# Optimization experiments

Measured on AMD Instinct MI355X. Metric: run time of the kernel, lower is better.

## Reference

```python
import jax, jax.numpy as jnp
import numpy as np

K = 3        # kernel size
PAD = 1      # padding
DG = 16      # deformable groups
MAXR = 10.0  # max_residue_magnitude


def _lrelu(x):
    return jnp.where(x >= 0, x, 0.1 * x)


def _conv3(x, w, b):
    y = jax.lax.conv_general_dilated(x, w, (1, 1), 'SAME',
                                     dimension_numbers=('NCHW', 'OIHW', 'NCHW'))
    return y + b[None, :, None, None]


def _deform_conv2d(x, offset, mask, weight, bias):
    # x: [B,Cin,H,W]; offset: [B,2*DG*K*K,H,W]; mask: [B,DG*K*K,H,W]
    B, Cin, H, W = x.shape
    Cout = weight.shape[0]
    G, Cg, K2 = DG, Cin // DG, K * K
    off = offset.reshape(B, G, K2, 2, H, W)
    dy, dx = off[:, :, :, 0], off[:, :, :, 1]
    ky = jnp.repeat(jnp.arange(K), K).astype(x.dtype)   # [K2]
    kx = jnp.tile(jnp.arange(K), K).astype(x.dtype)
    hh = jnp.arange(H, dtype=x.dtype)
    ww = jnp.arange(W, dtype=x.dtype)
    # sampling positions [B,G,K2,H,W]
    py = dy + ky[None, None, :, None, None] + hh[None, None, None, :, None] - PAD
    px = dx + kx[None, None, :, None, None] + ww[None, None, None, None, :] - PAD
    y0 = jnp.floor(py)
    x0 = jnp.floor(px)
    wy1 = py - y0
    wx1 = px - x0
    xf = x.reshape(B, G, Cg, H * W)

    def gather(yi, xi, wgt):
        valid = (yi >= 0) & (yi <= H - 1) & (xi >= 0) & (xi <= W - 1)
        idx = (jnp.clip(yi, 0, H - 1).astype(jnp.int32) * W
               + jnp.clip(xi, 0, W - 1).astype(jnp.int32)).reshape(B, G, -1)
        vals = jnp.take_along_axis(
            xf, jnp.broadcast_to(idx[:, :, None, :], (B, G, Cg, idx.shape[-1])), axis=3)
        vals = vals.reshape(B, G, Cg, K2, H, W)
        w = (wgt * valid.astype(x.dtype))[:, :, None]  # [B,G,1,K2,H,W]
        return vals * w

    s = (gather(y0, x0, (1 - wy1) * (1 - wx1))
         + gather(y0, x0 + 1, (1 - wy1) * wx1)
         + gather(y0 + 1, x0, wy1 * (1 - wx1))
         + gather(y0 + 1, x0 + 1, wy1 * wx1))
    s = s * mask.reshape(B, G, K2, H, W)[:, :, None]
    wr = weight.reshape(Cout, G, Cg, K2)
    out = jnp.einsum('ogck,bgckhw->bohw', wr, s)
    return out + bias[None, :, None, None]


def setup_inputs() -> dict:
    key = jax.random.key(0)
    ks = jax.random.split(key, 16)
    B, Cin, Cout, H, W = 4, 128, 64, 96, 96
    Coff = 3 * Cout + 4  # 196
    stdv = 1.0 / np.sqrt(Cin * K * K)
    inp = {
        'x': jax.random.normal(ks[0], (B, Cin, H, W), jnp.float32),
        'extra_feat': jax.random.normal(ks[1], (B, 3 * Cout, H, W), jnp.float32),
        'flow_1': jax.random.normal(ks[2], (B, 2, H, W), jnp.float32),
        'flow_2': jax.random.normal(ks[3], (B, 2, H, W), jnp.float32),
        'weight': jax.random.uniform(ks[4], (Cout, Cin, K, K), jnp.float32, -stdv, stdv),
        'bias': jax.random.normal(ks[5], (Cout,), jnp.float32) * 0.01,
        'ow0': jax.random.normal(ks[6], (Cout, Coff, K, K), jnp.float32) * 0.02,
        'ob0': jnp.zeros((Cout,), jnp.float32),
        'ow1': jax.random.normal(ks[7], (Cout, Cout, K, K), jnp.float32) * 0.02,
        'ob1': jnp.zeros((Cout,), jnp.float32),
        'ow2': jax.random.normal(ks[8], (Cout, Cout, K, K), jnp.float32) * 0.02,
        'ob2': jnp.zeros((Cout,), jnp.float32),
        'ow3': jax.random.normal(ks[9], (27 * DG, Cout, K, K), jnp.float32) * 0.01,
        'ob3': jnp.zeros((27 * DG,), jnp.float32),
    }
    return inp


def reference(x, extra_feat, flow_1, flow_2, weight, bias,
              ow0, ob0, ow1, ob1, ow2, ob2, ow3, ob3):
    feat = jnp.concatenate([extra_feat, flow_1, flow_2], axis=1)
    h = _lrelu(_conv3(feat, ow0, ob0))
    h = _lrelu(_conv3(h, ow1, ob1))
    h = _lrelu(_conv3(h, ow2, ob2))
    out = _conv3(h, ow3, ob3)
    o1, o2, m = jnp.split(out, 3, axis=1)
    offs = MAXR * jnp.tanh(jnp.concatenate([o1, o2], axis=1))
    off1, off2 = jnp.split(offs, 2, axis=1)
    off1 = off1 + jnp.tile(flow_1[:, ::-1], (1, off1.shape[1] // 2, 1, 1))
    off2 = off2 + jnp.tile(flow_2[:, ::-1], (1, off2.shape[1] // 2, 1, 1))
    offset = jnp.concatenate([off1, off2], axis=1)
    mask = jax.nn.sigmoid(m)
    return _deform_conv2d(x, offset, mask, weight, bias)
```

## Files before the change

kernel.cpp:

```cpp
#include <hip/hip_runtime.h>
#include <math.h>

#define HW 9216
#define Hh 96
#define Ww 96
#define PHW 9604

typedef __attribute__((ext_vector_type(8))) short bh8;
typedef __attribute__((ext_vector_type(4))) short bh4;
typedef __attribute__((ext_vector_type(4))) float f32x4;
typedef __attribute__((ext_vector_type(2))) float f32x2;
typedef __attribute__((ext_vector_type(4))) int i32x4;
union bh8i { bh8 v; i32x4 i; };

__device__ __forceinline__ short f2bf(float f) {
    union { float f; unsigned u; } v; v.f = f;
    unsigned r = v.u + 0x7FFFu + ((v.u >> 16) & 1u);
    return (short)(r >> 16);
}
__device__ __forceinline__ float bf2f(short s) {
    union { unsigned u; float f; } v; v.u = ((unsigned)(unsigned short)s) << 16;
    return v.f;
}
__device__ __forceinline__ float lo_bf(unsigned u) {
    union { unsigned u; float f; } v; v.u = u << 16; return v.f;
}
__device__ __forceinline__ float hi_bf(unsigned u) {
    union { unsigned u; float f; } v; v.u = u & 0xFFFF0000u; return v.f;
}
__device__ __forceinline__ unsigned pack_bf2(float lo, float hi) {
    union { float f; unsigned u; } a, b; a.f = lo; b.f = hi;
    unsigned ul = a.u + 0x7FFFu + ((a.u >> 16) & 1u);
    unsigned uh = b.u + 0x7FFFu + ((b.u >> 16) & 1u);
    return (ul >> 16) | (uh & 0xFFFF0000u);
}

__global__ void prep_misc(short* __restrict__ xpad1, short* __restrict__ hpa,
                          short* __restrict__ hpb, short* __restrict__ xdp,
                          const float* __restrict__ ow0, const float* __restrict__ ow1,
                          const float* __restrict__ ow2, const float* __restrict__ ow3,
                          const float* __restrict__ wd,
                          short* __restrict__ wb0, short* __restrict__ wb1,
                          short* __restrict__ wb2, short* __restrict__ wb3,
                          short* __restrict__ wbd) {
    int i = blockIdx.x * 256 + threadIdx.x;
    const int z1 = 4 * 388 * 224, z2 = 4 * 388 * 64;
    if (i < z1 + 2 * z2) {
        short* p; int C;
        if (i < z1) { p = xpad1; C = 224; }
        else if (i < z1 + z2) { p = hpa; C = 64; i -= z1; }
        else { p = hpb; C = 64; i -= z1 + z2; }
        int c = i % C;
        int r = i / C;
        int b = r / 388, pid = r - b * 388;
        int row, col;
        if (pid < 98)       { row = 0;  col = pid; }
        else if (pid < 196) { row = 97; col = pid - 98; }
        else if (pid < 292) { row = pid - 196 + 1; col = 0; }
        else                { row = pid - 292 + 1; col = 97; }
        p[((size_t)b * PHW + row * 98 + col) * C + c] = 0;
        return;
    }
    i -= z1 + 2 * z2;
    const int zr = 4 * 16 * 388 * 8;
    if (i < zr) {
        int c8 = i & 7;
        int r = i >> 3;
        int pid = r % 388;
        int bg = r / 388;
        int row, col;
        if (pid < 98)       { row = 0;  col = pid; }
        else if (pid < 196) { row = 97; col = pid - 98; }
        else if (pid < 292) { row = pid - 196 + 1; col = 0; }
        else                { row = pid - 292 + 1; col = 97; }
        xdp[((size_t)bg * PHW + row * 98 + col) * 8 + c8] = 0;
        return;
    }
    i -= zr;
    const int n0 = 64 * 9 * 224, n1 = 64 * 9 * 64, n3 = 448 * 9 * 64, nd = 64 * 1152;
    if (i < n0) {
        int co = i / (9 * 224); int r = i - co * (9 * 224);
        int tap = r / 224, ci = r - tap * 224;
        wb0[i] = f2bf(ci < 196 ? ow0[(co * 196 + ci) * 9 + tap] : 0.f);
        return;
    }
    i -= n0;
    if (i < n1) {
        int co = i / (9 * 64); int r = i - co * (9 * 64);
        int tap = r / 64, ci = r - tap * 64;
        wb1[i] = f2bf(ow1[(co * 64 + ci) * 9 + tap]);
        return;
    }
    i -= n1;
    if (i < n1) {
        int co = i / (9 * 64); int r = i - co * (9 * 64);
        int tap = r / 64, ci = r - tap * 64;
        wb2[i] = f2bf(ow2[(co * 64 + ci) * 9 + tap]);
        return;
    }
    i -= n1;
    if (i < n3) {
        int co = i / (9 * 64); int r = i - co * (9 * 64);
        int tap = r / 64, ci = r - tap * 64;
        wb3[i] = f2bf(co < 432 ? ow3[(co * 64 + ci) * 9 + tap] : 0.f);
        return;
    }
    i -= n3;
    if (i < nd) {
        int co = i / 1152, kd = i - co * 1152;
        int gt = kd >> 3, c = kd & 7;
        int g = gt / 9, tap = gt - g * 9;
        wbd[i] = f2bf(wd[(co * 128 + g * 8 + c) * 9 + tap]);
    }
}

__global__ void pack_all(const float* __restrict__ extra,
                         const float* __restrict__ f1,
                         const float* __restrict__ f2,
                         const float* __restrict__ x,
                         short* __restrict__ xp,
                         short* __restrict__ xdp) {
    __shared__ float t[32][33];
    const int tid = threadIdx.x, tx = tid & 31, ty = tid >> 5;
    const int pt = blockIdx.x, b = blockIdx.z;
    if (blockIdx.y < 7) {
        const int ct = blockIdx.y;
#pragma unroll
        for (int j = 0; j < 4; ++j) {
            int ch = ct * 32 + ty + j * 8;
            int p = pt * 32 + tx;
            float v = 0.f;
            if (ch < 192)      v = extra[(b * 192 + ch) * HW + p];
            else if (ch < 194) v = f1[(b * 2 + ch - 192) * HW + p];
            else if (ch < 196) v = f2[(b * 2 + ch - 194) * HW + p];
            t[ty + j * 8][tx] = v;
        }
        __syncthreads();
#pragma unroll
        for (int j = 0; j < 4; ++j) {
            int pr = ty + j * 8;
            int p = pt * 32 + pr;
            int r = p / 96, c = p - r * 96;
            xp[((size_t)b * PHW + (r + 1) * 98 + (c + 1)) * 224 + ct * 32 + tx] =
                f2bf(t[tx][pr]);
        }
    } else {
        const int ct = blockIdx.y - 7;
#pragma unroll
        for (int j = 0; j < 4; ++j) {
            int ch = ct * 32 + ty + j * 8;
            t[ty + j * 8][tx] = x[((size_t)b * 128 + ch) * HW + pt * 32 + tx];
        }
        __syncthreads();
        if (tid < 128) {
            int oct = tid >> 5, p = tid & 31;
            int g = ct * 4 + oct;
            int pix = pt * 32 + p;
            int r = pix / 96, c = pix - r * 96;
            bh8 v;
#pragma unroll
            for (int cc = 0; cc < 8; ++cc) v[cc] = f2bf(t[oct * 8 + cc][p]);
            *(bh8*)&xdp[(((size_t)b * 16 + g) * PHW + (r + 1) * 98 + (c + 1)) * 8] = v;
        }
    }
}

template<int CINP, int KCH>
__launch_bounds__(256)
__global__ void conv_mfma(const short* __restrict__ xp,
                          const short* __restrict__ wb,
                          const float* __restrict__ bias,
                          short* __restrict__ o1) {
    __shared__ __attribute__((aligned(16))) short smA[9 * 64 * 32];
    const int tid = threadIdx.x;
    const int lane = tid & 63, wv = tid >> 6;
    const int q = lane >> 4, l15 = lane & 15;
    const int b = blockIdx.y;
    const int pix0 = blockIdx.x * 64 + wv * 16;
    const int soh = pix0 / 96, sow = pix0 - (pix0 / 96) * 96;

    const short* bp = xp + ((size_t)b * PHW + soh * 98 + sow + l15) * CINP + q * 8;

    const int sco = tid >> 2, sqq = tid & 3;
    const short* wsrc = wb + (size_t)sco * (9 * CINP) + sqq * 8;

    f32x4 acc[4];
#pragma unroll
    for (int t = 0; t < 4; ++t) acc[t] = (f32x4){0.f, 0.f, 0.f, 0.f};

    for (int p = 0; p < KCH; ++p) {
        __syncthreads();
        bh8 wtmp[9];
#pragma unroll
        for (int tap = 0; tap < 9; ++tap)
            wtmp[tap] = *(const bh8*)(wsrc + tap * CINP + p * 32);
#pragma unroll
        for (int tap = 0; tap < 9; ++tap)
            *(bh8*)&smA[tap * 2048 + sco * 32 + sqq * 8] = wtmp[tap];
        __syncthreads();
#pragma unroll
        for (int tap = 0; tap < 9; ++tap) {
            const int ky = tap / 3, kx = tap - (tap / 3) * 3;
            bh8 bf = *(const bh8*)(bp + (ky * 98 + kx) * CINP + p * 32);
#pragma unroll
            for (int t = 0; t < 4; ++t) {
                bh8 af = *(const bh8*)&smA[tap * 2048 + (t * 16 + l15) * 32 + q * 8];
                acc[t] = __builtin_amdgcn_mfma_f32_16x16x32_bf16(af, bf, acc[t], 0, 0, 0);
            }
        }
    }

    size_t base = ((size_t)b * PHW + (soh + 1) * 98 + sow + l15 + 1) * 64;
#pragma unroll
    for (int t = 0; t < 4; ++t) {
        bh4 v4;
#pragma unroll
        for (int r = 0; r < 4; ++r) {
            int co = t * 16 + q * 4 + r;
            float v = acc[t][r] + bias[co];
            v = (v >= 0.f) ? v : 0.1f * v;
            v4[r] = f2bf(v);
        }
        *(bh4*)(o1 + base + t * 16 + q * 4) = v4;
    }
}

__launch_bounds__(256)
__global__ void conv4_gemm(const short* __restrict__ xp,
                           const short* __restrict__ wb,
                           const float* __restrict__ bias,
                           float* __restrict__ offp,
                           short* __restrict__ maskb,
                           const float* __restrict__ flow1,
                           const float* __restrict__ flow2) {
    __shared__ __attribute__((aligned(16))) short smA[64 * 64];
    __shared__ __attribute__((aligned(16))) short smB[192 * 64];
    const int tid = threadIdx.x;
    const int lane = tid & 63, wv = tid >> 6;
    const int q = lane >> 4, l15 = lane & 15;
    const int pg = blockIdx.x;
    const int b = blockIdx.y;
    const int cob = blockIdx.z * 64;
    const int r0 = pg * 2;

    f32x4 acc[3][4];
#pragma unroll
    for (int pf = 0; pf < 3; ++pf)
#pragma unroll
        for (int cf = 0; cf < 4; ++cf) acc[pf][cf] = (f32x4){0.f, 0.f, 0.f, 0.f};

    for (int tap = 0; tap < 9; ++tap) {
        const int ky = tap / 3, kx = tap - (tap / 3) * 3;
        __syncthreads();
#pragma unroll
        for (int it = 0; it < 2; ++it) {
            int id = it * 256 + tid;
            int row = id >> 3, s = id & 7;
            int sw = s ^ (row & 7);
            *(bh8*)&smA[row * 64 + sw * 8] =
                *(const bh8*)(wb + (size_t)(cob + row) * 576 + tap * 64 + s * 8);
        }
#pragma unroll
        for (int it = 0; it < 6; ++it) {
            int id = it * 256 + tid;
            int row = id >> 3, s = id & 7;
            int sw = s ^ (row & 7);
            int srow = (row >= 96) ? 1 : 0;
            int scol = row - srow * 96;
            *(bh8*)&smB[row * 64 + sw * 8] = *(const bh8*)&xp[
                ((size_t)b * PHW + (r0 + srow + ky) * 98 + scol + kx) * 64 + s * 8];
        }
        __syncthreads();
#pragma unroll
        for (int kc = 0; kc < 2; ++kc) {
            bh8 bf[3], af[4];
#pragma unroll
            for (int pf = 0; pf < 3; ++pf) {
                int row = wv * 48 + pf * 16 + l15;
                int sw = (kc * 4 + q) ^ (row & 7);
                bf[pf] = *(const bh8*)&smB[row * 64 + sw * 8];
            }
#pragma unroll
            for (int cf = 0; cf < 4; ++cf) {
                int row = cf * 16 + l15;
                int sw = (kc * 4 + q) ^ (row & 7);
                af[cf] = *(const bh8*)&smA[row * 64 + sw * 8];
            }
#pragma unroll
            for (int pf = 0; pf < 3; ++pf)
#pragma unroll
                for (int cf = 0; cf < 4; ++cf)
                    acc[pf][cf] = __builtin_amdgcn_mfma_f32_16x16x32_bf16(
                        af[cf], bf[pf], acc[pf][cf], 0, 0, 0);
        }
    }

#pragma unroll
    for (int pf = 0; pf < 3; ++pf) {
        int local = wv * 48 + pf * 16 + l15;
        int lrow = (local >= 96) ? 1 : 0;
        int pix = (r0 + lrow) * 96 + (local - lrow * 96);
#pragma unroll
        for (int cf = 0; cf < 4; ++cf) {
            int cb0 = cob + cf * 16 + q * 4;
            if (cb0 < 288) {
                const float* fl = (cb0 < 144) ? flow1 : flow2;
                float fe = fl[(b * 2 + 1) * HW + pix];
                float fo = fl[(b * 2) * HW + pix];
                float t0 = 10.f * tanhf(acc[pf][cf][0] + bias[cb0 + 0]) + fe;
                float t1 = 10.f * tanhf(acc[pf][cf][1] + bias[cb0 + 1]) + fo;
                float t2 = 10.f * tanhf(acc[pf][cf][2] + bias[cb0 + 2]) + fe;
                float t3 = 10.f * tanhf(acc[pf][cf][3] + bias[cb0 + 3]) + fo;
                size_t p0 = ((size_t)b * 144 + (cb0 >> 1)) * HW + pix;
                *(f32x2*)&offp[p0 * 2] = (f32x2){t0, t1};
                *(f32x2*)&offp[(p0 + HW) * 2] = (f32x2){t2, t3};
            } else {
#pragma unroll
                for (int r = 0; r < 4; ++r) {
                    int chn = cb0 + r;
                    if (chn < 432) {
                        float v = acc[pf][cf][r] + bias[chn];
                        maskb[((size_t)b * 144 + (chn - 288)) * HW + pix] =
                            f2bf(1.f / (1.f + expf(-v)));
                    }
                }
            }
        }
    }
}

__launch_bounds__(256)
__global__ void deform_mfma(const short* __restrict__ xdp,
                            const float* __restrict__ offp,
                            const short* __restrict__ maskb,
                            const short* __restrict__ wbd,
                            const float* __restrict__ bias,
                            float* __restrict__ out) {
    __shared__ float red[4][1024];
    const int tid = threadIdx.x;
    const int lane = tid & 63, wv = tid >> 6;
    const int q = lane >> 4, l15 = lane & 15;
    const int blk = blockIdx.x;
    const int xs = blk & 7, idx = blk >> 3;
    const int b = xs >> 1;
    const int pix0 = ((xs & 1) * 288 + idx) * 16;
    const int pix = pix0 + l15;
    const int h = pix / 96, w = pix - (pix / 96) * 96;

    const float* opp = offp + ((size_t)b * 144 * HW + pix) * 2;
    const short* mp = maskb + (size_t)b * 144 * HW + pix;
    const short* xb = xdp + (size_t)b * 16 * PHW * 8;
    const short* ap = wbd + (size_t)l15 * 1152 + wv * 288 + q * 8;

    f32x2 dxy[9];
    float mk[9];
#pragma unroll
    for (int i = 0; i < 9; ++i) {
        const int gt = wv * 36 + i * 4 + q;
        dxy[i] = *(const f32x2*)(opp + (size_t)gt * HW * 2);
        mk[i] = bf2f(mp[(size_t)gt * HW]);
    }

    const short* cp[9];
    f32x4 ww[9];
#pragma unroll
    for (int i = 0; i < 9; ++i) {
        const int gt = wv * 36 + i * 4 + q;
        const int g = gt / 9, tap = gt - (gt / 9) * 9;
        float py = dxy[i][0] + (float)(tap / 3) + (float)h - 1.f;
        float px = dxy[i][1] + (float)(tap - (tap / 3) * 3) + (float)w - 1.f;
        py = fminf(fmaxf(py, -1.f), 96.f);
        px = fminf(fmaxf(px, -1.f), 96.f);
        float y0f = floorf(py), x0f = floorf(px);
        float wy1 = py - y0f, wx1 = px - x0f;
        float wy0 = 1.f - wy1, wx0 = 1.f - wx1;
        int yp = (int)y0f + 1, xp = (int)x0f + 1;
        cp[i] = xb + ((size_t)g * PHW + yp * 98 + xp) * 8;
        float m = mk[i];
        ww[i] = (f32x4){wy0 * wx0 * m, wy0 * wx1 * m, wy1 * wx0 * m, wy1 * wx1 * m};
    }

    f32x4 acc[4];
#pragma unroll
    for (int t = 0; t < 4; ++t) acc[t] = (f32x4){0.f, 0.f, 0.f, 0.f};

#pragma unroll
    for (int i = 0; i < 9; ++i) {
        bh8i c00, c01, c10, c11;
        c00.v = *(const bh8*)(cp[i]);
        c01.v = *(const bh8*)(cp[i] + 8);
        c10.v = *(const bh8*)(cp[i] + 98 * 8);
        c11.v = *(const bh8*)(cp[i] + 99 * 8);
        const float w00 = ww[i][0], w01 = ww[i][1], w10 = ww[i][2], w11 = ww[i][3];
        bh8i bf;
#pragma unroll
        for (int k = 0; k < 4; ++k) {
            unsigned u00 = (unsigned)c00.i[k], u01 = (unsigned)c01.i[k];
            unsigned u10 = (unsigned)c10.i[k], u11 = (unsigned)c11.i[k];
            float lo = w00 * lo_bf(u00) + w01 * lo_bf(u01)
                     + w10 * lo_bf(u10) + w11 * lo_bf(u11);
            float hi = w00 * hi_bf(u00) + w01 * hi_bf(u01)
                     + w10 * hi_bf(u10) + w11 * hi_bf(u11);
            bf.i[k] = (int)pack_bf2(lo, hi);
        }
#pragma unroll
        for (int t = 0; t < 4; ++t) {
            bh8 af = *(const bh8*)(ap + (size_t)t * 16 * 1152 + i * 32);
            acc[t] = __builtin_amdgcn_mfma_f32_16x16x32_bf16(af, bf.v, acc[t], 0, 0, 0);
        }
    }

#pragma unroll
    for (int t = 0; t < 4; ++t)
#pragma unroll
        for (int r = 0; r < 4; ++r)
            red[wv][(t * 16 + q * 4 + r) * 16 + l15] = acc[t][r];
    __syncthreads();
    for (int e = tid; e < 1024; e += 256) {
        int co = e >> 4, pl = e & 15;
        float v = red[0][e] + red[1][e] + red[2][e] + red[3][e] + bias[co];
        out[((size_t)b * 64 + co) * HW + pix0 + pl] = v;
    }
}

extern "C" void kernel_launch(void* const* d_in, const int* in_sizes, int n_in,
                              void* d_out, int out_size, void* d_ws, size_t ws_size,
                              hipStream_t stream) {
    const float* x      = (const float*)d_in[0];
    const float* extra  = (const float*)d_in[1];
    const float* flow1  = (const float*)d_in[2];
    const float* flow2  = (const float*)d_in[3];
    const float* weight = (const float*)d_in[4];
    const float* bias   = (const float*)d_in[5];
    const float* ow0    = (const float*)d_in[6];
    const float* ob0    = (const float*)d_in[7];
    const float* ow1    = (const float*)d_in[8];
    const float* ob1    = (const float*)d_in[9];
    const float* ow2    = (const float*)d_in[10];
    const float* ob2    = (const float*)d_in[11];
    const float* ow3    = (const float*)d_in[12];
    const float* ob3    = (const float*)d_in[13];
    float* out = (float*)d_out;

    char* wsb = (char*)d_ws;
    short* xpad1 = (short*)wsb;   wsb += (size_t)4 * PHW * 224 * 2;
    short* hpa   = (short*)wsb;   wsb += (size_t)4 * PHW * 64 * 2;
    short* hpb   = (short*)wsb;   wsb += (size_t)4 * PHW * 64 * 2;
    float* offpair = (float*)wsb; wsb += (size_t)4 * 144 * HW * 2 * 4;
    short* maskbuf = (short*)wsb; wsb += (size_t)4 * 144 * HW * 2;
    short* xdp     = (short*)wsb; wsb += (size_t)4 * 16 * PHW * 8 * 2 + 32;
    short* wb0     = (short*)wsb; wsb += 64 * 9 * 224 * 2;
    short* wb1     = (short*)wsb; wsb += 64 * 9 * 64 * 2;
    short* wb2     = (short*)wsb; wsb += 64 * 9 * 64 * 2;
    short* wb3     = (short*)wsb; wsb += 448 * 9 * 64 * 2;
    short* wbd     = (short*)wsb;

    const int prep_total = 546304 + 198656 + 534528;
    prep_misc<<<dim3((prep_total + 255) / 256), 256, 0, stream>>>(
        xpad1, hpa, hpb, xdp, ow0, ow1, ow2, ow3, weight,
        wb0, wb1, wb2, wb3, wbd);
    pack_all<<<dim3(288, 11, 4), 256, 0, stream>>>(extra, flow1, flow2, x, xpad1, xdp);

    conv_mfma<224, 7><<<dim3(144, 4), 256, 0, stream>>>(xpad1, wb0, ob0, hpa);
    conv_mfma<64, 2><<<dim3(144, 4), 256, 0, stream>>>(hpa, wb1, ob1, hpb);
    conv_mfma<64, 2><<<dim3(144, 4), 256, 0, stream>>>(hpb, wb2, ob2, hpa);
    conv4_gemm<<<dim3(48, 4, 7), 256, 0, stream>>>(hpa, wb3, ob3, offpair,
                                                   maskbuf, flow1, flow2);
    deform_mfma<<<dim3(2304), 256, 0, stream>>>(xdp, offpair, maskbuf, wbd, bias, out);
}
```

Before: 291.4 us.

## Restructure offset conv GEMM to full-Cout blocks and prefetch weights in registers

The final offset/mask conv now has each block cover all 448 output channels for 64 pixels, with B fragments read straight from global memory. Previously the grid tiled 64 output channels by 192 pixels, so the input activations were reloaded into shared memory once per channel tile. Weights are staged through padded shared memory in 32-channel chunks, and the next chunk is prefetched into registers. The same register prefetch is added to the earlier conv kernel. This cuts redundant activation traffic and hides weight-load latency, at the cost of a large accumulator array (28 f32x4) that raises register pressure and may lower occupancy.

```diff
diff --git a/kernel.cpp b/kernel.cpp
--- a/kernel.cpp
+++ b/kernel.cpp
@@ -188,16 +188,22 @@
 #pragma unroll
     for (int t = 0; t < 4; ++t) acc[t] = (f32x4){0.f, 0.f, 0.f, 0.f};
 
+    bh8 wtmp[9];
+#pragma unroll
+    for (int tap = 0; tap < 9; ++tap)
+        wtmp[tap] = *(const bh8*)(wsrc + tap * CINP);
+
     for (int p = 0; p < KCH; ++p) {
         __syncthreads();
-        bh8 wtmp[9];
-#pragma unroll
-        for (int tap = 0; tap < 9; ++tap)
-            wtmp[tap] = *(const bh8*)(wsrc + tap * CINP + p * 32);
 #pragma unroll
         for (int tap = 0; tap < 9; ++tap)
             *(bh8*)&smA[tap * 2048 + sco * 32 + sqq * 8] = wtmp[tap];
         __syncthreads();
+        if (p + 1 < KCH) {
+#pragma unroll
+            for (int tap = 0; tap < 9; ++tap)
+                wtmp[tap] = *(const bh8*)(wsrc + tap * CINP + (p + 1) * 32);
+        }
 #pragma unroll
         for (int tap = 0; tap < 9; ++tap) {
             const int ky = tap / 3, kx = tap - (tap / 3) * 3;
@@ -233,96 +239,89 @@
                            short* __restrict__ maskb,
                            const float* __restrict__ flow1,
                            const float* __restrict__ flow2) {
-    __shared__ __attribute__((aligned(16))) short smA[64 * 64];
-    __shared__ __attribute__((aligned(16))) short smB[192 * 64];
+    __shared__ __attribute__((aligned(16))) short smA[448 * 40];
     const int tid = threadIdx.x;
     const int lane = tid & 63, wv = tid >> 6;
     const int q = lane >> 4, l15 = lane & 15;
-    const int pg = blockIdx.x;
     const int b = blockIdx.y;
-    const int cob = blockIdx.z * 64;
-    const int r0 = pg * 2;
-
-    f32x4 acc[3][4];
-#pragma unroll
-    for (int pf = 0; pf < 3; ++pf)
-#pragma unroll
-        for (int cf = 0; cf < 4; ++cf) acc[pf][cf] = (f32x4){0.f, 0.f, 0.f, 0.f};
-
-    for (int tap = 0; tap < 9; ++tap) {
+    const int pix0 = blockIdx.x * 64;
+
+    int soh[4], sow[4];
+    const short* bp[4];
+#pragma unroll
+    for (int s = 0; s < 4; ++s) {
+        int pixs = pix0 + s * 16;
+        soh[s] = pixs / 96;
+        sow[s] = pixs - soh[s] * 96;
+        bp[s] = xp + ((size_t)b * PHW + soh[s] * 98 + sow[s] + l15) * 64 + q * 8;
+    }
+
+    const int srow = tid >> 2, ssl = tid & 3;
+    const short* asrc = wb + (size_t)srow * 576 + ssl * 8;
+
+    f32x4 acc[7][4];
+#pragma unroll
+    for (int cf = 0; cf < 7; ++cf)
+#pragma unroll
+        for (int s = 0; s < 4; ++s) acc[cf][s] = (f32x4){0.f, 0.f, 0.f, 0.f};
+
+    bh8 wtmp[7];
+#pragma unroll
+    for (int it = 0; it < 7; ++it)
+        wtmp[it] = *(const bh8*)(asrc + (size_t)it * 64 * 576);
+
+    for (int ch = 0; ch < 18; ++ch) {
+        const int tap = ch >> 1, ci = (ch & 1) * 32;
         const int ky = tap / 3, kx = tap - (tap / 3) * 3;
         __syncthreads();
 #pragma unroll
-        for (int it = 0; it < 2; ++it) {
-            int id = it * 256 + tid;
-            int row = id >> 3, s = id & 7;
-            int sw = s ^ (row & 7);
-            *(bh8*)&smA[row * 64 + sw * 8] =
-                *(const bh8*)(wb + (size_t)(cob + row) * 576 + tap * 64 + s * 8);
-        }
-#pragma unroll
-        for (int it = 0; it < 6; ++it) {
-            int id = it * 256 + tid;
-            int row = id >> 3, s = id & 7;
-            int sw = s ^ (row & 7);
-            int srow = (row >= 96) ? 1 : 0;
-            int scol = row - srow * 96;
-            *(bh8*)&smB[row * 64 + sw * 8] = *(const bh8*)&xp[
-                ((size_t)b * PHW + (r0 + srow + ky) * 98 + scol + kx) * 64 + s * 8];
-        }
-        __syncthreads();
-#pragma unroll
-        for (int kc = 0; kc < 2; ++kc) {
-            bh8 bf[3], af[4];
-#pragma unroll
-            for (int pf = 0; pf < 3; ++pf) {
-                int row = wv * 48 + pf * 16 + l15;
-                int sw = (kc * 4 + q) ^ (row & 7);
-                bf[pf] = *(const bh8*)&smB[row * 64 + sw * 8];
-            }
-#pragma unroll
-            for (int cf = 0; cf < 4; ++cf) {
-                int row = cf * 16 + l15;
-                int sw = (kc * 4 + q) ^ (row & 7);
-                af[cf] = *(const bh8*)&smA[row * 64 + sw * 8];
-            }
-#pragma unroll
-            for (int pf = 0; pf < 3; ++pf)
-#pragma unroll
-                for (int cf = 0; cf < 4; ++cf)
-                    acc[pf][cf] = __builtin_amdgcn_mfma_f32_16x16x32_bf16(
-                        af[cf], bf[pf], acc[pf][cf], 0, 0, 0);
-        }
-    }
-
-#pragma unroll
-    for (int pf = 0; pf < 3; ++pf) {
-        int local = wv * 48 + pf * 16 + l15;
-        int lrow = (local >= 96) ? 1 : 0;
-        int pix = (r0 + lrow) * 96 + (local - lrow * 96);
-#pragma unroll
-        for (int cf = 0; cf < 4; ++cf) {
-            int cb0 = cob + cf * 16 + q * 4;
+        for (int it = 0; it < 7; ++it)
+            *(bh8*)&smA[(srow + it * 64) * 40 + ssl * 8] = wtmp[it];
+        __syncthreads();
+        if (ch + 1 < 18) {
+            const int ntap = (ch + 1) >> 1, nci = ((ch + 1) & 1) * 32;
+#pragma unroll
+            for (int it = 0; it < 7; ++it)
+                wtmp[it] = *(const bh8*)(asrc + (size_t)it * 64 * 576 + ntap * 64 + nci);
+        }
+        bh8 bf[4];
+#pragma unroll
+        for (int s = 0; s < 4; ++s)
+            bf[s] = *(const bh8*)(bp[s] + (ky * 98 + kx) * 64 + ci);
+#pragma unroll
+        for (int cf = 0; cf < 7; ++cf) {
+            bh8 af = *(const bh8*)&smA[(wv * 112 + cf * 16 + l15) * 40 + q * 8];
+#pragma unroll
+            for (int s = 0; s < 4; ++s)
+                acc[cf][s] = __builtin_amdgcn_mfma_f32_16x16x32_bf16(
+                    af, bf[s], acc[cf][s], 0, 0, 0);
+        }
+    }
+
+#pragma unroll
+    for (int s = 0; s < 4; ++s) {
+        int pix = pix0 + s * 16 + l15;
+#pragma unroll
+        for (int cf = 0; cf < 7; ++cf) {
+            int cb0 = wv * 112 + cf * 16 + q * 4;
             if (cb0 < 288) {
                 const float* fl = (cb0 < 144) ? flow1 : flow2;
                 float fe = fl[(b * 2 + 1) * HW + pix];
                 float fo = fl[(b * 2) * HW + pix];
-                float t0 = 10.f * tanhf(acc[pf][cf][0] + bias[cb0 + 0]) + fe;
-                float t1 = 10.f * tanhf(acc[pf][cf][1] + bias[cb0 + 1]) + fo;
-                float t2 = 10.f * tanhf(acc[pf][cf][2] + bias[cb0 + 2]) + fe;
-                float t3 = 10.f * tanhf(acc[pf][cf][3] + bias[cb0 + 3]) + fo;
+                float t0 = 10.f * tanhf(acc[cf][s][0] + bias[cb0 + 0]) + fe;
+                float t1 = 10.f * tanhf(acc[cf][s][1] + bias[cb0 + 1]) + fo;
+                float t2 = 10.f * tanhf(acc[cf][s][2] + bias[cb0 + 2]) + fe;
+                float t3 = 10.f * tanhf(acc[cf][s][3] + bias[cb0 + 3]) + fo;
                 size_t p0 = ((size_t)b * 144 + (cb0 >> 1)) * HW + pix;
                 *(f32x2*)&offp[p0 * 2] = (f32x2){t0, t1};
                 *(f32x2*)&offp[(p0 + HW) * 2] = (f32x2){t2, t3};
-            } else {
+            } else if (cb0 < 432) {
 #pragma unroll
                 for (int r = 0; r < 4; ++r) {
                     int chn = cb0 + r;
-                    if (chn < 432) {
-                        float v = acc[pf][cf][r] + bias[chn];
-                        maskb[((size_t)b * 144 + (chn - 288)) * HW + pix] =
-                            f2bf(1.f / (1.f + expf(-v)));
-                    }
+                    float v = acc[cf][s][r] + bias[chn];
+                    maskb[((size_t)b * 144 + (chn - 288)) * HW + pix] =
+                        f2bf(1.f / (1.f + expf(-v)));
                 }
             }
         }
@@ -464,7 +463,7 @@
     conv_mfma<224, 7><<<dim3(144, 4), 256, 0, stream>>>(xpad1, wb0, ob0, hpa);
     conv_mfma<64, 2><<<dim3(144, 4), 256, 0, stream>>>(hpa, wb1, ob1, hpb);
     conv_mfma<64, 2><<<dim3(144, 4), 256, 0, stream>>>(hpb, wb2, ob2, hpa);
-    conv4_gemm<<<dim3(48, 4, 7), 256, 0, stream>>>(hpa, wb3, ob3, offpair,
-                                                   maskbuf, flow1, flow2);
+    conv4_gemm<<<dim3(144, 4), 256, 0, stream>>>(hpa, wb3, ob3, offpair,
+                                                 maskbuf, flow1, flow2);
     deform_mfma<<<dim3(2304), 256, 0, stream>>>(xdp, offpair, maskbuf, wbd, bias, out);
 }
```

New measurement: 369.0 us. 26.6% more time.

## Load conv4 activation fragments directly from global memory instead of LDS staging

Applied to the files above, without the earlier changes.

The conv4 GEMM kernel no longer stages the 192-pixel activation tile into shared memory each tap. Each lane now computes per-subtile base pointers into the padded input and reads its MFMA B fragments straight from global memory, so pixel subtiles can span row boundaries. This removes the LDS store/load traffic and shrinks shared memory, which may raise occupancy. In exchange, global reads are repeated across taps and the four column-block blocks with no LDS reuse, relying on the cache.

```diff
diff --git a/kernel.cpp b/kernel.cpp
--- a/kernel.cpp
+++ b/kernel.cpp
@@ -234,20 +234,26 @@
                            const float* __restrict__ flow1,
                            const float* __restrict__ flow2) {
     __shared__ __attribute__((aligned(16))) short smA[64 * 64];
-    __shared__ __attribute__((aligned(16))) short smB[192 * 64];
     const int tid = threadIdx.x;
     const int lane = tid & 63, wv = tid >> 6;
     const int q = lane >> 4, l15 = lane & 15;
-    const int pg = blockIdx.x;
     const int b = blockIdx.y;
     const int cob = blockIdx.z * 64;
-    const int r0 = pg * 2;
-
-    f32x4 acc[3][4];
-#pragma unroll
-    for (int pf = 0; pf < 3; ++pf)
-#pragma unroll
-        for (int cf = 0; cf < 4; ++cf) acc[pf][cf] = (f32x4){0.f, 0.f, 0.f, 0.f};
+    const int pixw = blockIdx.x * 192 + wv * 48;
+
+    const short* bp[3];
+#pragma unroll
+    for (int s = 0; s < 3; ++s) {
+        int pixs = pixw + s * 16;
+        int soh = pixs / 96, sow = pixs - (pixs / 96) * 96;
+        bp[s] = xp + ((size_t)b * PHW + soh * 98 + sow + l15) * 64 + q * 8;
+    }
+
+    f32x4 acc[4][3];
+#pragma unroll
+    for (int cf = 0; cf < 4; ++cf)
+#pragma unroll
+        for (int s = 0; s < 3; ++s) acc[cf][s] = (f32x4){0.f, 0.f, 0.f, 0.f};
 
     for (int tap = 0; tap < 9; ++tap) {
         const int ky = tap / 3, kx = tap - (tap / 3) * 3;
@@ -260,26 +266,13 @@
             *(bh8*)&smA[row * 64 + sw * 8] =
                 *(const bh8*)(wb + (size_t)(cob + row) * 576 + tap * 64 + s * 8);
         }
-#pragma unroll
-        for (int it = 0; it < 6; ++it) {
-            int id = it * 256 + tid;
-            int row = id >> 3, s = id & 7;
-            int sw = s ^ (row & 7);
-            int srow = (row >= 96) ? 1 : 0;
-            int scol = row - srow * 96;
-            *(bh8*)&smB[row * 64 + sw * 8] = *(const bh8*)&xp[
-                ((size_t)b * PHW + (r0 + srow + ky) * 98 + scol + kx) * 64 + s * 8];
-        }
         __syncthreads();
 #pragma unroll
         for (int kc = 0; kc < 2; ++kc) {
             bh8 bf[3], af[4];
 #pragma unroll
-            for (int pf = 0; pf < 3; ++pf) {
-                int row = wv * 48 + pf * 16 + l15;
-                int sw = (kc * 4 + q) ^ (row & 7);
-                bf[pf] = *(const bh8*)&smB[row * 64 + sw * 8];
-            }
+            for (int s = 0; s < 3; ++s)
+                bf[s] = *(const bh8*)(bp[s] + (ky * 98 + kx) * 64 + kc * 32);
 #pragma unroll
             for (int cf = 0; cf < 4; ++cf) {
                 int row = cf * 16 + l15;
@@ -287,19 +280,17 @@
                 af[cf] = *(const bh8*)&smA[row * 64 + sw * 8];
             }
 #pragma unroll
-            for (int pf = 0; pf < 3; ++pf)
-#pragma unroll
-                for (int cf = 0; cf < 4; ++cf)
-                    acc[pf][cf] = __builtin_amdgcn_mfma_f32_16x16x32_bf16(
-                        af[cf], bf[pf], acc[pf][cf], 0, 0, 0);
-        }
-    }
-
-#pragma unroll
-    for (int pf = 0; pf < 3; ++pf) {
-        int local = wv * 48 + pf * 16 + l15;
-        int lrow = (local >= 96) ? 1 : 0;
-        int pix = (r0 + lrow) * 96 + (local - lrow * 96);
+            for (int cf = 0; cf < 4; ++cf)
+#pragma unroll
+                for (int s = 0; s < 3; ++s)
+                    acc[cf][s] = __builtin_amdgcn_mfma_f32_16x16x32_bf16(
+                        af[cf], bf[s], acc[cf][s], 0, 0, 0);
+        }
+    }
+
+#pragma unroll
+    for (int s = 0; s < 3; ++s) {
+        int pix = pixw + s * 16 + l15;
 #pragma unroll
         for (int cf = 0; cf < 4; ++cf) {
             int cb0 = cob + cf * 16 + q * 4;
@@ -307,10 +298,10 @@
                 const float* fl = (cb0 < 144) ? flow1 : flow2;
                 float fe = fl[(b * 2 + 1) * HW + pix];
                 float fo = fl[(b * 2) * HW + pix];
-                float t0 = 10.f * tanhf(acc[pf][cf][0] + bias[cb0 + 0]) + fe;
-                float t1 = 10.f * tanhf(acc[pf][cf][1] + bias[cb0 + 1]) + fo;
-                float t2 = 10.f * tanhf(acc[pf][cf][2] + bias[cb0 + 2]) + fe;
-                float t3 = 10.f * tanhf(acc[pf][cf][3] + bias[cb0 + 3]) + fo;
+                float t0 = 10.f * tanhf(acc[cf][s][0] + bias[cb0 + 0]) + fe;
+                float t1 = 10.f * tanhf(acc[cf][s][1] + bias[cb0 + 1]) + fo;
+                float t2 = 10.f * tanhf(acc[cf][s][2] + bias[cb0 + 2]) + fe;
+                float t3 = 10.f * tanhf(acc[cf][s][3] + bias[cb0 + 3]) + fo;
                 size_t p0 = ((size_t)b * 144 + (cb0 >> 1)) * HW + pix;
                 *(f32x2*)&offp[p0 * 2] = (f32x2){t0, t1};
                 *(f32x2*)&offp[(p0 + HW) * 2] = (f32x2){t2, t3};
@@ -319,7 +310,7 @@
                 for (int r = 0; r < 4; ++r) {
                     int chn = cb0 + r;
                     if (chn < 432) {
-                        float v = acc[pf][cf][r] + bias[chn];
+                        float v = acc[cf][s][r] + bias[chn];
                         maskb[((size_t)b * 144 + (chn - 288)) * HW + pix] =
                             f2bf(1.f / (1.f + expf(-v)));
                     }
```

New measurement: 313.8 us. +7.7%, slower.
